# Kernel tuning notes

Hardware: AMD Instinct MI355X
Metric: run time of the kernel (lower is better)

## Reference

```python
import jax, jax.numpy as jnp
import numpy as np

B, T, N, M, P = 1024, 128, 128, 256, 256


def _lstm_step(x, h, c, Wih, Whh, bih, bhh):
    # PyTorch LSTM cell: gates ordered i, f, g, o
    g = x @ Wih.T + bih + h @ Whh.T + bhh
    i, f, gg, o = jnp.split(g, 4, axis=-1)
    c_new = jax.nn.sigmoid(f) * c + jax.nn.sigmoid(i) * jnp.tanh(gg)
    h_new = jax.nn.sigmoid(o) * jnp.tanh(c_new)
    return h_new, c_new


def darnn_forward(enc_data, dec_data, enc_Wih, enc_Whh, enc_bih, enc_bhh,
                  We, Ue, ve, Wd, Ud, vd, wt_w, wt_b,
                  dec_Wih, dec_Whh, dec_bih, dec_bhh, l1_w, l1_b, l2_w, l2_b):
    Bsz, Tlen, n = enc_data.shape
    m = enc_Whh.shape[1]
    p = dec_Whh.shape[1]
    # ---- Encoder with input attention ----
    # U_e(data.permute(0,2,1)): (B, n, T); constant across time steps
    Ue_data = jnp.einsum('btn,st->bns', enc_data, Ue)
    def enc_step(carry, x_t):
        h, c = carry                                   # (B, m) each
        q = jnp.concatenate([h, c], axis=-1)           # (B, 2m)
        wq = q @ We.T                                  # (B, T)
        score = jnp.tanh(wq[:, None, :] + Ue_data) @ ve  # (B, n)
        alpha = jax.nn.softmax(score, axis=-1)
        h, c = _lstm_step(alpha * x_t, h, c, enc_Wih, enc_Whh, enc_bih, enc_bhh)
        return (h, c), h
    h0 = jnp.zeros((Bsz, m), enc_data.dtype)
    (_, _), Hs = jax.lax.scan(enc_step, (h0, h0), jnp.swapaxes(enc_data, 0, 1))
    H = jnp.swapaxes(Hs, 0, 1)                         # (B, T, m)
    # ---- Decoder with temporal attention ----
    UH = jnp.einsum('btm,um->btu', H, Ud)              # (B, T, m); constant
    def attn_ctx(d, s):
        q = jnp.concatenate([d, s], axis=-1)           # (B, 2p)
        wq = q @ Wd.T                                  # (B, m)
        score = jnp.tanh(wq[:, None, :] + UH) @ vd     # (B, T)
        beta = jax.nn.softmax(score, axis=-1)
        return jnp.einsum('bt,btm->bm', beta, H)       # (B, m)
    def dec_step(carry, y):
        d, s = carry
        ctx = attn_ctx(d, s)
        y_tilde = jnp.concatenate([y, ctx], axis=-1) @ wt_w.T + wt_b  # (B, 1)
        d, s = _lstm_step(y_tilde, d, s, dec_Wih, dec_Whh, dec_bih, dec_bhh)
        return (d, s), None
    d0 = jnp.zeros((Bsz, p), enc_data.dtype)
    ys = jnp.swapaxes(dec_data[:, :Tlen - 1, :], 0, 1)  # (T-1, B, 1)
    (d, s), _ = jax.lax.scan(dec_step, (d0, d0), ys)
    ctx = attn_ctx(d, s)
    out = jnp.concatenate([d, ctx], axis=-1)            # (B, p + m)
    out = jax.nn.relu(out @ l1_w.T + l1_b) @ l2_w.T + l2_b
    return out.reshape(-1)


def setup_inputs() -> dict:
    key = jax.random.key(0)
    ks = jax.random.split(key, 22)
    f = lambda k, shape: jax.random.normal(k, shape, jnp.float32) * 0.05
    return {
        'enc_data': jax.random.normal(ks[0], (B, T, N), jnp.float32),
        'dec_data': jax.random.normal(ks[1], (B, T, 1), jnp.float32),
        'enc_Wih': f(ks[2], (4 * M, N)), 'enc_Whh': f(ks[3], (4 * M, M)),
        'enc_bih': f(ks[4], (4 * M,)), 'enc_bhh': f(ks[5], (4 * M,)),
        'We': f(ks[6], (T, 2 * M)), 'Ue': f(ks[7], (T, T)), 've': f(ks[8], (T,)),
        'Wd': f(ks[9], (M, 2 * P)), 'Ud': f(ks[10], (M, M)), 'vd': f(ks[11], (M,)),
        'wt_w': f(ks[12], (1, M + 1)), 'wt_b': f(ks[13], (1,)),
        'dec_Wih': f(ks[14], (4 * P, 1)), 'dec_Whh': f(ks[15], (4 * P, P)),
        'dec_bih': f(ks[16], (4 * P,)), 'dec_bhh': f(ks[17], (4 * P,)),
        'l1_w': f(ks[18], (P, M + P)), 'l1_b': f(ks[19], (P,)),
        'l2_w': f(ks[20], (1, P)), 'l2_b': f(ks[21], (1,)),
    }


def reference(enc_data, dec_data, enc_Wih, enc_Whh, enc_bih, enc_bhh,
              We, Ue, ve, Wd, Ud, vd, wt_w, wt_b,
              dec_Wih, dec_Whh, dec_bih, dec_bhh, l1_w, l1_b, l2_w, l2_b):
    return darnn_forward(enc_data, dec_data, enc_Wih, enc_Whh, enc_bih, enc_bhh,
                         We, Ue, ve, Wd, Ud, vd, wt_w, wt_b,
                         dec_Wih, dec_Whh, dec_bih, dec_bhh, l1_w, l1_b, l2_w, l2_b)
```

## Files before the change

### kernel.cpp

```cpp
#include <hip/hip_runtime.h>

typedef unsigned short ushort_t;
typedef unsigned char u8_t;
typedef float f32x2 __attribute__((ext_vector_type(2)));

static constexpr int BATCH = 1024;
static constexpr int TT = 128;
static constexpr int NN = 128;
static constexpr int MM = 256;

__device__ __forceinline__ float bf2f(ushort_t u) {
    union { unsigned int i; float f; } v;
    v.i = ((unsigned int)u) << 16;
    return v.f;
}
__device__ __forceinline__ ushort_t f2bf(float f) {
    union { unsigned int i; float f; } v;
    v.f = f;
    unsigned int i = v.i;
    return (ushort_t)((i + 0x7FFFu + ((i >> 16) & 1u)) >> 16);
}
__device__ __forceinline__ void unp8(const int4 w, float* o) {
    union { unsigned int i; float f; } v;
    v.i = ((unsigned int)w.x) << 16;        o[0] = v.f;
    v.i = ((unsigned int)w.x) & 0xffff0000u; o[1] = v.f;
    v.i = ((unsigned int)w.y) << 16;        o[2] = v.f;
    v.i = ((unsigned int)w.y) & 0xffff0000u; o[3] = v.f;
    v.i = ((unsigned int)w.z) << 16;        o[4] = v.f;
    v.i = ((unsigned int)w.z) & 0xffff0000u; o[5] = v.f;
    v.i = ((unsigned int)w.w) << 16;        o[6] = v.f;
    v.i = ((unsigned int)w.w) & 0xffff0000u; o[7] = v.f;
}
__device__ __forceinline__ void unp4(const int2 w, float* o) {
    union { unsigned int i; float f; } v;
    v.i = ((unsigned int)w.x) << 16;        o[0] = v.f;
    v.i = ((unsigned int)w.x) & 0xffff0000u; o[1] = v.f;
    v.i = ((unsigned int)w.y) << 16;        o[2] = v.f;
    v.i = ((unsigned int)w.y) & 0xffff0000u; o[3] = v.f;
}
__device__ __forceinline__ void unp8f8(const int2 w, float* o) {
    f32x2 a = __builtin_amdgcn_cvt_pk_f32_fp8(w.x, false);
    f32x2 b = __builtin_amdgcn_cvt_pk_f32_fp8(w.x, true);
    f32x2 c = __builtin_amdgcn_cvt_pk_f32_fp8(w.y, false);
    f32x2 d = __builtin_amdgcn_cvt_pk_f32_fp8(w.y, true);
    o[0] = a.x; o[1] = a.y; o[2] = b.x; o[3] = b.y;
    o[4] = c.x; o[5] = c.y; o[6] = d.x; o[7] = d.y;
}
__device__ __forceinline__ float tanh_fast(float x) {
    float e = __expf(2.0f * x);
    return 1.0f - __fdividef(2.0f, e + 1.0f);
}
__device__ __forceinline__ float sig_fast(float x) {
    return __fdividef(1.0f, 1.0f + __expf(-x));
}

template<bool WBF16, bool TRANSW, int CMODE, bool RELU>
__global__ __launch_bounds__(256) void gemm_k(
    const float* __restrict__ A1, int lda1, long sA1z, int K1,
    const float* __restrict__ A2, int lda2, int K2,
    const void* __restrict__ W1v, int ldw1, long sW1z,
    const void* __restrict__ W2v, int ldw2,
    const float* __restrict__ bias1,
    void* __restrict__ Cv, int ldc, long sCz)
{
    __shared__ float As[32][68];
    __shared__ float Ws[32][68];
    const int tid = threadIdx.x;
    const int z = blockIdx.z;
    const int m0 = blockIdx.y * 64;
    const int g0 = blockIdx.x * 64;
    const int tm = tid & 15, tn = tid >> 4;
    float acc[4][4];
#pragma unroll
    for (int i = 0; i < 4; ++i)
#pragma unroll
        for (int j = 0; j < 4; ++j) acc[i][j] = 0.0f;

    for (int phase = 0; phase < 2; ++phase) {
        const float* A = (phase == 0) ? (A1 + (long)z * sA1z) : A2;
        const int lda = (phase == 0) ? lda1 : lda2;
        const int K = (phase == 0) ? K1 : K2;
        const int ldw = (phase == 0) ? ldw1 : ldw2;
        const void* Wv = (phase == 0) ? W1v : W2v;
        const long woff = (phase == 0) ? (long)z * sW1z : 0;
        if (A == nullptr || Wv == nullptr || K <= 0) continue;

        for (int k0 = 0; k0 < K; k0 += 32) {
            const int rem = K - k0;
            {
                const int tr0 = tid >> 3;
                const int tk = (tid & 7) * 4;
#pragma unroll
                for (int pass = 0; pass < 2; ++pass) {
                    const int m = tr0 + pass * 32;
                    const float* p = A + (long)(m0 + m) * lda + k0 + tk;
#pragma unroll
                    for (int j = 0; j < 4; ++j) {
                        float v = 0.0f;
                        if (tk + j < rem) v = p[j];
                        As[tk + j][m] = v;
                    }
                }
            }
            if constexpr (TRANSW) {
                const float* W = (const float*)Wv + woff;
                const int gq = (tid & 15) * 4;
                const int kr = tid >> 4;
#pragma unroll
                for (int pass = 0; pass < 2; ++pass) {
                    const int k = kr + pass * 16;
                    const float* p = W + (long)(k0 + k) * ldw + g0 + gq;
                    const bool ok = (k < rem);
#pragma unroll
                    for (int j = 0; j < 4; ++j) {
                        float v = 0.0f;
                        if (ok) v = p[j];
                        Ws[k][gq + j] = v;
                    }
                }
            } else if constexpr (WBF16) {
                const ushort_t* W = (const ushort_t*)Wv + woff;
                const int g = tid >> 2;
                const int tk = (tid & 3) * 8;
                const ushort_t* p = W + (long)(g0 + g) * ldw + k0 + tk;
#pragma unroll
                for (int j = 0; j < 8; ++j) {
                    float v = 0.0f;
                    if (tk + j < rem) v = bf2f(p[j]);
                    Ws[tk + j][g] = v;
                }
            } else {
                const float* W = (const float*)Wv + woff;
                const int tr0 = tid >> 3;
                const int tk = (tid & 7) * 4;
#pragma unroll
                for (int pass = 0; pass < 2; ++pass) {
                    const int g = tr0 + pass * 32;
                    const float* p = W + (long)(g0 + g) * ldw + k0 + tk;
#pragma unroll
                    for (int j = 0; j < 4; ++j) {
                        float v = 0.0f;
                        if (tk + j < rem) v = p[j];
                        Ws[tk + j][g] = v;
                    }
                }
            }
            __syncthreads();
#pragma unroll
            for (int kk = 0; kk < 32; ++kk) {
                const float4 av = *(const float4*)&As[kk][tm * 4];
                const float4 bv = *(const float4*)&Ws[kk][tn * 4];
                const float a[4] = {av.x, av.y, av.z, av.w};
                const float b[4] = {bv.x, bv.y, bv.z, bv.w};
#pragma unroll
                for (int i = 0; i < 4; ++i)
#pragma unroll
                    for (int j = 0; j < 4; ++j)
                        acc[i][j] = fmaf(a[i], b[j], acc[i][j]);
            }
            __syncthreads();
        }
    }
#pragma unroll
    for (int i = 0; i < 4; ++i) {
        const long m = m0 + tm * 4 + i;
        if constexpr (CMODE == 2) {
            float v[4];
#pragma unroll
            for (int j = 0; j < 4; ++j) {
                v[j] = acc[i][j];
                if (bias1) v[j] += bias1[g0 + tn * 4 + j];
                if (RELU) v[j] = fmaxf(v[j], 0.0f);
            }
            int pk = __builtin_amdgcn_cvt_pk_fp8_f32(v[0], v[1], 0, false);
            pk = __builtin_amdgcn_cvt_pk_fp8_f32(v[2], v[3], pk, true);
            *(unsigned int*)((u8_t*)Cv + (long)z * sCz + m * ldc + g0 + tn * 4) =
                (unsigned int)pk;
        } else {
#pragma unroll
            for (int j = 0; j < 4; ++j) {
                const int g = g0 + tn * 4 + j;
                float v = acc[i][j];
                if (bias1) v += bias1[g];
                if (RELU) v = fmaxf(v, 0.0f);
                if constexpr (CMODE == 1)
                    ((ushort_t*)Cv)[(long)z * sCz + m * ldc + g] = f2bf(v);
                else
                    ((float*)Cv)[(long)z * sCz + m * ldc + g] = v;
            }
        }
    }
}

__global__ void prep_encw_k(const float* __restrict__ Wih, const float* __restrict__ Whh,
                            ushort_t* __restrict__ dst) {
    int i = blockIdx.x * 256 + threadIdx.x;
    if (i >= 384 * 1024) return;
    int k = i >> 10, col = i & 1023, u = col >> 2, q = col & 3, g = q * 256 + u;
    float v = (k < 128) ? Wih[g * 128 + k] : Whh[g * 256 + (k - 128)];
    dst[(k >> 1) * 2048 + u * 8 + (k & 1) * 4 + q] = f2bf(v);
}

__global__ void prep_decw_k(const float* __restrict__ Wih, const float* __restrict__ Whh,
                            ushort_t* __restrict__ dst) {
    int i = blockIdx.x * 256 + threadIdx.x;
    if (i >= 257 * 1024) return;
    int k = i >> 10, col = i & 1023, u = col >> 2, q = col & 3, g = q * 256 + u;
    float v = (k == 0) ? Wih[g] : Whh[g * 256 + (k - 1)];
    ushort_t b = f2bf(v);
    if (k == 0) {
        dst[col] = b;
    } else {
        int kk = k - 1;
        dst[1024 + (kk >> 1) * 2048 + u * 8 + (kk & 1) * 4 + q] = b;
    }
}

__global__ void transpose_k(const float* __restrict__ src, float* __restrict__ dst,
                            int R, int C) {
    int i = blockIdx.x * 256 + threadIdx.x;
    if (i < R * C) { int r = i / C, c = i - r * C; dst[c * R + r] = src[i]; }
}

__global__ void packT_k(const float* __restrict__ src, ushort_t* __restrict__ dst,
                        int R, int C) {
    int i = blockIdx.x * 256 + threadIdx.x;
    if (i >= R * C) return;
    int s = i / C, k = i - s * C;
    dst[(k >> 1) * (2 * R) + (s >> 2) * 8 + (k & 1) * 4 + (s & 3)] = f2bf(src[i]);
}

__global__ __launch_bounds__(512) void enc_persist(
    const float* __restrict__ enc_data,
    const u8_t* __restrict__ D,
    const ushort_t* __restrict__ WeB,
    const float* __restrict__ ve,
    const ushort_t* __restrict__ WencB,
    const float* __restrict__ bih, const float* __restrict__ bhh,
    ushort_t* __restrict__ Hbf)
{
    const int tid = threadIdx.x;
    const int b0 = blockIdx.x * 4;
    __shared__ __align__(16) float hs[256][4];
    __shared__ __align__(16) float cs[256][4];
    __shared__ __align__(16) float xt[128][4];
    __shared__ __align__(16) float wqp[16][128][4];
    __shared__ __align__(16) float wqs[128][4];
    __shared__ __align__(16) float scp[8][4][128];
    __shared__ float gp[4][4][256];
    __shared__ float ves[128];

    if (tid < 128) ves[tid] = ve[tid];
    if (tid < 256) {
        const float4 z = make_float4(0.f, 0.f, 0.f, 0.f);
        *(float4*)hs[tid] = z;
        *(float4*)cs[tid] = z;
    }
    const int u = tid & 255;
    const int ks = tid >> 8;
    const float b_i = bih[u] + bhh[u];
    const float b_f = bih[256 + u] + bhh[256 + u];
    const float b_g = bih[512 + u] + bhh[512 + u];
    const float b_o = bih[768 + u] + bhh[768 + u];
    __syncthreads();

    const int kgq = tid >> 5, sv = tid & 31;
    const ushort_t* wq_w = WeB + (long)(kgq * 16) * 256 + sv * 8;
    const float* qbase = (kgq < 8) ? &hs[kgq * 32][0] : &cs[(kgq - 8) * 32][0];
    const int nv = tid & 15, srow = (tid >> 4) & 3, ssl = tid >> 6;
    const u8_t* Dp0 = D + (long)(b0 + srow) * 16384 + (ssl * 16) * 128 + nv * 8;
    const ushort_t* gw = WencB + u * 8;

    float SVe = 0.0f;
#pragma unroll
    for (int s = 0; s < 16; ++s) SVe += ves[ssl * 16 + s];

    for (int t = 0; t < 128; ++t) {
        {
            float a[4][4];
#pragma unroll
            for (int m = 0; m < 4; ++m)
#pragma unroll
                for (int r = 0; r < 4; ++r) a[m][r] = 0.0f;
#pragma unroll 4
            for (int k2 = 0; k2 < 16; ++k2) {
                const int4 wv = *(const int4*)(wq_w + k2 * 256);
                float w8[8]; unp8(wv, w8);
                const float4 q0 = *(const float4*)(qbase + (2 * k2) * 4);
                const float4 q1 = *(const float4*)(qbase + (2 * k2 + 1) * 4);
                const float qa0[4] = {q0.x, q0.y, q0.z, q0.w};
                const float qa1[4] = {q1.x, q1.y, q1.z, q1.w};
#pragma unroll
                for (int m = 0; m < 4; ++m)
#pragma unroll
                    for (int r = 0; r < 4; ++r)
                        a[m][r] = fmaf(w8[4 + m], qa1[r], fmaf(w8[m], qa0[r], a[m][r]));
            }
#pragma unroll
            for (int m = 0; m < 4; ++m)
                *(float4*)wqp[kgq][sv * 4 + m] = make_float4(a[m][0], a[m][1], a[m][2], a[m][3]);
        }
        __syncthreads();
        if (tid < 128) {
            float4 s = *(const float4*)wqp[0][tid];
#pragma unroll
            for (int g = 1; g < 16; ++g) {
                const float4 p = *(const float4*)wqp[g][tid];
                s.x += p.x; s.y += p.y; s.z += p.z; s.w += p.w;
            }
            *(float4*)wqs[tid] = s;
        }
        __syncthreads();
        {
            float a[8];
#pragma unroll
            for (int j = 0; j < 8; ++j) a[j] = 0.0f;
#pragma unroll 4
            for (int s = 0; s < 16; ++s) {
                const int sg = ssl * 16 + s;
                const float w2 = wqs[sg][srow] * 2.0f;
                const float vv = ves[sg];
                const int2 wv2 = *(const int2*)(Dp0 + s * 128);
                float d[8];
                unp8f8(wv2, d);
#pragma unroll
                for (int j = 0; j < 8; ++j) {
                    const float ex = __expf(fmaf(d[j], 2.0f, w2));
                    a[j] = fmaf(vv, __fdividef(1.0f, ex + 1.0f), a[j]);
                }
            }
            *(float4*)&scp[ssl][srow][nv * 8] =
                make_float4(fmaf(-2.f, a[0], SVe), fmaf(-2.f, a[1], SVe),
                            fmaf(-2.f, a[2], SVe), fmaf(-2.f, a[3], SVe));
            *(float4*)&scp[ssl][srow][nv * 8 + 4] =
                make_float4(fmaf(-2.f, a[4], SVe), fmaf(-2.f, a[5], SVe),
                            fmaf(-2.f, a[6], SVe), fmaf(-2.f, a[7], SVe));
        }
        __syncthreads();
        if (tid < 256) {
            const int w = tid >> 6, lane = tid & 63;
            float s0 = 0.0f, s1 = 0.0f;
#pragma unroll
            for (int g = 0; g < 8; ++g) {
                s0 += scp[g][w][lane];
                s1 += scp[g][w][lane + 64];
            }
            float mx = fmaxf(s0, s1);
            for (int o = 32; o > 0; o >>= 1) mx = fmaxf(mx, __shfl_xor(mx, o, 64));
            const float e0 = __expf(s0 - mx), e1 = __expf(s1 - mx);
            float sm = e0 + e1;
            for (int o = 32; o > 0; o >>= 1) sm += __shfl_xor(sm, o, 64);
            const float inv = __fdividef(1.0f, sm);
            const float* xp = enc_data + ((long)(b0 + w) * 128 + t) * 128;
            xt[lane][w] = e0 * inv * xp[lane];
            xt[lane + 64][w] = e1 * inv * xp[lane + 64];
        }
        __syncthreads();
        float acc[4][4];
#pragma unroll
        for (int q = 0; q < 4; ++q)
#pragma unroll
            for (int r = 0; r < 4; ++r) acc[q][r] = 0.0f;
        if (ks == 0) {
#pragma unroll 4
            for (int p = 0; p < 64; ++p) {
                const int4 wv = *(const int4*)(gw + (long)p * 2048);
                float w8[8]; unp8(wv, w8);
                const float4 x0 = *(const float4*)xt[2 * p];
                const float4 x1 = *(const float4*)xt[2 * p + 1];
                const float xa0[4] = {x0.x, x0.y, x0.z, x0.w};
                const float xa1[4] = {x1.x, x1.y, x1.z, x1.w};
#pragma unroll
                for (int q = 0; q < 4; ++q)
#pragma unroll
                    for (int r = 0; r < 4; ++r)
                        acc[q][r] = fmaf(w8[4 + q], xa1[r], fmaf(w8[q], xa0[r], acc[q][r]));
            }
#pragma unroll 4
            for (int p = 64; p < 96; ++p) {
                const int4 wv = *(const int4*)(gw + (long)p * 2048);
                float w8[8]; unp8(wv, w8);
                const float4 x0 = *(const float4*)hs[2 * p - 128];
                const float4 x1 = *(const float4*)hs[2 * p - 127];
                const float xa0[4] = {x0.x, x0.y, x0.z, x0.w};
                const float xa1[4] = {x1.x, x1.y, x1.z, x1.w};
#pragma unroll
                for (int q = 0; q < 4; ++q)
#pragma unroll
                    for (int r = 0; r < 4; ++r)
                        acc[q][r] = fmaf(w8[4 + q], xa1[r], fmaf(w8[q], xa0[r], acc[q][r]));
            }
        } else {
#pragma unroll 4
            for (int p = 96; p < 192; ++p) {
                const int4 wv = *(const int4*)(gw + (long)p * 2048);
                float w8[8]; unp8(wv, w8);
                const float4 x0 = *(const float4*)hs[2 * p - 128];
                const float4 x1 = *(const float4*)hs[2 * p - 127];
                const float xa0[4] = {x0.x, x0.y, x0.z, x0.w};
                const float xa1[4] = {x1.x, x1.y, x1.z, x1.w};
#pragma unroll
                for (int q = 0; q < 4; ++q)
#pragma unroll
                    for (int r = 0; r < 4; ++r)
                        acc[q][r] = fmaf(w8[4 + q], xa1[r], fmaf(w8[q], xa0[r], acc[q][r]));
            }
#pragma unroll
            for (int q = 0; q < 4; ++q)
#pragma unroll
                for (int r = 0; r < 4; ++r) gp[q][r][u] = acc[q][r];
        }
        __syncthreads();
        if (ks == 0) {
#pragma unroll
            for (int r = 0; r < 4; ++r) {
                const float iv = sig_fast(acc[0][r] + gp[0][r][u] + b_i);
                const float fv = sig_fast(acc[1][r] + gp[1][r][u] + b_f);
                const float gv = tanh_fast(acc[2][r] + gp[2][r][u] + b_g);
                const float ov = sig_fast(acc[3][r] + gp[3][r][u] + b_o);
                const float cn = fv * cs[u][r] + iv * gv;
                const float hn = ov * tanh_fast(cn);
                cs[u][r] = cn;
                hs[u][r] = hn;
                Hbf[((long)(b0 + r) * 128 + t) * 256 + u] = f2bf(hn);
            }
        }
        __syncthreads();
    }
}

__global__ __launch_bounds__(512) void dec_persist(
    const float* __restrict__ dec_data,
    const u8_t* __restrict__ UH2,
    const ushort_t* __restrict__ Hb,
    const ushort_t* __restrict__ WdB,
    const float* __restrict__ vd,
    const ushort_t* __restrict__ WdecB,
    const float* __restrict__ bih, const float* __restrict__ bhh,
    const float* __restrict__ wt_w, const float* __restrict__ wt_b,
    const float* __restrict__ l1T,
    const float* __restrict__ l1_b,
    const float* __restrict__ l2_w, const float* __restrict__ l2_b,
    float* __restrict__ out)
{
    const int tid = threadIdx.x;
    const int b0 = blockIdx.x * 4;
    __shared__ __align__(16) float ds4[256][4];
    __shared__ __align__(16) float ss4[256][4];
    __shared__ __align__(16) float wqp[8][256][4];
    __shared__ __align__(16) float wqs[256][4];
    __shared__ __align__(16) float scp[8][4][128];
    __shared__ __align__(16) float beta[128][4];
    __shared__ __align__(16) float ctxp[4][4][256];
    __shared__ __align__(16) float ctx4[256][4];
    __shared__ float gp[4][4][256];
    __shared__ __align__(16) float o14[256][4];
    __shared__ float vds[256];
    __shared__ float wt1s[256];
    __shared__ float l2s[256];
    __shared__ __align__(16) float yts[4];

    const int u = tid & 255;
    const int ks = tid >> 8;
    if (tid < 256) {
        vds[tid] = vd[tid];
        wt1s[tid] = wt_w[1 + tid];
        l2s[tid] = l2_w[tid];
        const float4 z = make_float4(0.f, 0.f, 0.f, 0.f);
        *(float4*)ds4[tid] = z;
        *(float4*)ss4[tid] = z;
    }
    const float b_i = bih[u] + bhh[u];
    const float b_f = bih[256 + u] + bhh[256 + u];
    const float b_g = bih[512 + u] + bhh[512 + u];
    const float b_o = bih[768 + u] + bhh[768 + u];
    __syncthreads();

    const int kgq = tid >> 6, mv = tid & 63;
    const ushort_t* wq_w = WdB + (long)(kgq * 32) * 512 + mv * 8;
    const float* qbase = (kgq < 4) ? &ds4[kgq * 64][0] : &ss4[(kgq - 4) * 64][0];
    const int tv = tid & 15, srow = (tid >> 4) & 3, usl = tid >> 6;
    const u8_t* up0 = UH2 + ((long)(b0 + srow) * 256 + usl * 32) * 128 + tv * 8;
    const int mv8 = tid & 31, crow = (tid >> 5) & 3, ssl2 = tid >> 7;
    const ushort_t* hp0 = Hb + ((long)(b0 + crow) * 128 + ssl2 * 32) * 256 + mv8 * 8;
    const ushort_t* gwp = WdecB + 1024 + u * 8;

    float SVd = 0.0f;
#pragma unroll
    for (int s = 0; s < 32; ++s) SVd += vds[usl * 32 + s];

    for (int td = 0; td < 128; ++td) {
        {
            float a[4][4];
#pragma unroll
            for (int m = 0; m < 4; ++m)
#pragma unroll
                for (int r = 0; r < 4; ++r) a[m][r] = 0.0f;
#pragma unroll 4
            for (int k2 = 0; k2 < 32; ++k2) {
                const int4 wv = *(const int4*)(wq_w + k2 * 512);
                float w8[8]; unp8(wv, w8);
                const float4 q0 = *(const float4*)(qbase + (2 * k2) * 4);
                const float4 q1 = *(const float4*)(qbase + (2 * k2 + 1) * 4);
                const float qa0[4] = {q0.x, q0.y, q0.z, q0.w};
                const float qa1[4] = {q1.x, q1.y, q1.z, q1.w};
#pragma unroll
                for (int m = 0; m < 4; ++m)
#pragma unroll
                    for (int r = 0; r < 4; ++r)
                        a[m][r] = fmaf(w8[4 + m], qa1[r], fmaf(w8[m], qa0[r], a[m][r]));
            }
#pragma unroll
            for (int m = 0; m < 4; ++m)
                *(float4*)wqp[kgq][mv * 4 + m] = make_float4(a[m][0], a[m][1], a[m][2], a[m][3]);
        }
        __syncthreads();
        if (tid < 256) {
            float4 s = *(const float4*)wqp[0][tid];
#pragma unroll
            for (int g = 1; g < 8; ++g) {
                const float4 p = *(const float4*)wqp[g][tid];
                s.x += p.x; s.y += p.y; s.z += p.z; s.w += p.w;
            }
            *(float4*)wqs[tid] = s;
        }
        __syncthreads();
        {
            float a[8];
#pragma unroll
            for (int j = 0; j < 8; ++j) a[j] = 0.0f;
#pragma unroll 4
            for (int uu = 0; uu < 32; ++uu) {
                const int ug = usl * 32 + uu;
                const float w2 = wqs[ug][srow] * 2.0f;
                const float vv = vds[ug];
                const int2 wv2 = *(const int2*)(up0 + uu * 128);
                float d[8];
                unp8f8(wv2, d);
#pragma unroll
                for (int j = 0; j < 8; ++j) {
                    const float ex = __expf(fmaf(d[j], 2.0f, w2));
                    a[j] = fmaf(vv, __fdividef(1.0f, ex + 1.0f), a[j]);
                }
            }
            *(float4*)&scp[usl][srow][tv * 8] =
                make_float4(fmaf(-2.f, a[0], SVd), fmaf(-2.f, a[1], SVd),
                            fmaf(-2.f, a[2], SVd), fmaf(-2.f, a[3], SVd));
            *(float4*)&scp[usl][srow][tv * 8 + 4] =
                make_float4(fmaf(-2.f, a[4], SVd), fmaf(-2.f, a[5], SVd),
                            fmaf(-2.f, a[6], SVd), fmaf(-2.f, a[7], SVd));
        }
        __syncthreads();
        if (tid < 256) {
            const int w = tid >> 6, lane = tid & 63;
            float s0 = 0.0f, s1 = 0.0f;
#pragma unroll
            for (int g = 0; g < 8; ++g) {
                s0 += scp[g][w][lane];
                s1 += scp[g][w][lane + 64];
            }
            float mx = fmaxf(s0, s1);
            for (int o = 32; o > 0; o >>= 1) mx = fmaxf(mx, __shfl_xor(mx, o, 64));
            const float e0 = __expf(s0 - mx), e1 = __expf(s1 - mx);
            float sm = e0 + e1;
            for (int o = 32; o > 0; o >>= 1) sm += __shfl_xor(sm, o, 64);
            const float inv = __fdividef(1.0f, sm);
            beta[lane][w] = e0 * inv;
            beta[lane + 64][w] = e1 * inv;
        }
        __syncthreads();
        {
            float c[8];
#pragma unroll
            for (int j = 0; j < 8; ++j) c[j] = 0.0f;
#pragma unroll 4
            for (int s = 0; s < 32; ++s) {
                const float bt = beta[ssl2 * 32 + s][crow];
                const int4 wv2 = *(const int4*)(hp0 + s * 256);
                float hv[8];
                unp8(wv2, hv);
#pragma unroll
                for (int j = 0; j < 8; ++j)
                    c[j] = fmaf(bt, hv[j], c[j]);
            }
            *(float4*)&ctxp[ssl2][crow][mv8 * 8]     = make_float4(c[0], c[1], c[2], c[3]);
            *(float4*)&ctxp[ssl2][crow][mv8 * 8 + 4] = make_float4(c[4], c[5], c[6], c[7]);
        }
        __syncthreads();
        if (tid < 256) {
            const int m = tid;
            float cr[4];
#pragma unroll
            for (int r = 0; r < 4; ++r)
                cr[r] = ctxp[0][r][m] + ctxp[1][r][m] + ctxp[2][r][m] + ctxp[3][r][m];
            *(float4*)ctx4[m] = make_float4(cr[0], cr[1], cr[2], cr[3]);
        }
        __syncthreads();
        if (td == 127) break;
        if (tid < 256) {
            const int w = tid >> 6, lane = tid & 63;
            float s = ctx4[lane][w] * wt1s[lane]
                    + ctx4[lane + 64][w] * wt1s[lane + 64]
                    + ctx4[lane + 128][w] * wt1s[lane + 128]
                    + ctx4[lane + 192][w] * wt1s[lane + 192];
            for (int o = 32; o > 0; o >>= 1) s += __shfl_xor(s, o, 64);
            if (lane == 0)
                yts[w] = s + wt_b[0] + wt_w[0] * dec_data[(long)(b0 + w) * 128 + td];
        }
        __syncthreads();
        float acc[4][4];
        if (ks == 0) {
            const int2 yv = *(const int2*)(WdecB + u * 4);
            float wy[4]; unp4(yv, wy);
            const float4 y4 = *(const float4*)yts;
            const float ya[4] = {y4.x, y4.y, y4.z, y4.w};
#pragma unroll
            for (int q = 0; q < 4; ++q)
#pragma unroll
                for (int r = 0; r < 4; ++r) acc[q][r] = wy[q] * ya[r];
#pragma unroll 4
            for (int p = 0; p < 64; ++p) {
                const int4 wv = *(const int4*)(gwp + (long)p * 2048);
                float w8[8]; unp8(wv, w8);
                const float4 x0 = *(const float4*)ds4[2 * p];
                const float4 x1 = *(const float4*)ds4[2 * p + 1];
                const float xa0[4] = {x0.x, x0.y, x0.z, x0.w};
                const float xa1[4] = {x1.x, x1.y, x1.z, x1.w};
#pragma unroll
                for (int q = 0; q < 4; ++q)
#pragma unroll
                    for (int r = 0; r < 4; ++r)
                        acc[q][r] = fmaf(w8[4 + q], xa1[r], fmaf(w8[q], xa0[r], acc[q][r]));
            }
        } else {
#pragma unroll
            for (int q = 0; q < 4; ++q)
#pragma unroll
                for (int r = 0; r < 4; ++r) acc[q][r] = 0.0f;
#pragma unroll 4
            for (int p = 64; p < 128; ++p) {
                const int4 wv = *(const int4*)(gwp + (long)p * 2048);
                float w8[8]; unp8(wv, w8);
                const float4 x0 = *(const float4*)ds4[2 * p];
                const float4 x1 = *(const float4*)ds4[2 * p + 1];
                const float xa0[4] = {x0.x, x0.y, x0.z, x0.w};
                const float xa1[4] = {x1.x, x1.y, x1.z, x1.w};
#pragma unroll
                for (int q = 0; q < 4; ++q)
#pragma unroll
                    for (int r = 0; r < 4; ++r)
                        acc[q][r] = fmaf(w8[4 + q], xa1[r], fmaf(w8[q], xa0[r], acc[q][r]));
            }
#pragma unroll
            for (int q = 0; q < 4; ++q)
#pragma unroll
                for (int r = 0; r < 4; ++r) gp[q][r][u] = acc[q][r];
        }
        __syncthreads();
        if (ks == 0) {
#pragma unroll
            for (int r = 0; r < 4; ++r) {
                const float iv = sig_fast(acc[0][r] + gp[0][r][u] + b_i);
                const float fv = sig_fast(acc[1][r] + gp[1][r][u] + b_f);
                const float gv = tanh_fast(acc[2][r] + gp[2][r][u] + b_g);
                const float ov = sig_fast(acc[3][r] + gp[3][r][u] + b_o);
                const float sn = fv * ss4[u][r] + iv * gv;
                const float dn = ov * tanh_fast(sn);
                ss4[u][r] = sn;
                ds4[u][r] = dn;
            }
        }
        __syncthreads();
    }
    {
        const float* src = l1T + ks * 256 * 256;
        float a0 = 0, a1 = 0, a2 = 0, a3 = 0;
#pragma unroll 4
        for (int k = 0; k < 256; ++k) {
            const float w = src[k * 256 + u];
            const float4 q = (ks == 0) ? *(const float4*)ds4[k]
                                       : *(const float4*)ctx4[k];
            a0 = fmaf(q.x, w, a0); a1 = fmaf(q.y, w, a1);
            a2 = fmaf(q.z, w, a2); a3 = fmaf(q.w, w, a3);
        }
        if (ks == 1) {
            gp[0][0][u] = a0; gp[0][1][u] = a1; gp[0][2][u] = a2; gp[0][3][u] = a3;
        } else {
            gp[1][0][u] = a0; gp[1][1][u] = a1; gp[1][2][u] = a2; gp[1][3][u] = a3;
        }
    }
    __syncthreads();
    if (tid < 256) {
        const float bb = l1_b[tid];
        *(float4*)o14[tid] = make_float4(
            fmaxf(gp[0][0][tid] + gp[1][0][tid] + bb, 0.f),
            fmaxf(gp[0][1][tid] + gp[1][1][tid] + bb, 0.f),
            fmaxf(gp[0][2][tid] + gp[1][2][tid] + bb, 0.f),
            fmaxf(gp[0][3][tid] + gp[1][3][tid] + bb, 0.f));
    }
    __syncthreads();
    if (tid < 256) {
        const int w = tid >> 6, lane = tid & 63;
        float s = o14[lane][w] * l2s[lane]
                + o14[lane + 64][w] * l2s[lane + 64]
                + o14[lane + 128][w] * l2s[lane + 128]
                + o14[lane + 192][w] * l2s[lane + 192];
        for (int o = 32; o > 0; o >>= 1) s += __shfl_xor(s, o, 64);
        if (lane == 0) out[b0 + w] = s + l2_b[0];
    }
}

extern "C" void kernel_launch(void* const* d_in, const int* in_sizes, int n_in,
                              void* d_out, int out_size, void* d_ws, size_t ws_size,
                              hipStream_t stream)
{
    const float* enc_data = (const float*)d_in[0];
    const float* dec_data = (const float*)d_in[1];
    const float* enc_Wih  = (const float*)d_in[2];
    const float* enc_Whh  = (const float*)d_in[3];
    const float* enc_bih  = (const float*)d_in[4];
    const float* enc_bhh  = (const float*)d_in[5];
    const float* We   = (const float*)d_in[6];
    const float* Ue   = (const float*)d_in[7];
    const float* ve   = (const float*)d_in[8];
    const float* Wd   = (const float*)d_in[9];
    const float* Ud   = (const float*)d_in[10];
    const float* vd   = (const float*)d_in[11];
    const float* wt_w = (const float*)d_in[12];
    const float* wt_b = (const float*)d_in[13];
    const float* dec_Wih = (const float*)d_in[14];
    const float* dec_Whh = (const float*)d_in[15];
    const float* dec_bih = (const float*)d_in[16];
    const float* dec_bhh = (const float*)d_in[17];
    const float* l1_w = (const float*)d_in[18];
    const float* l1_b = (const float*)d_in[19];
    const float* l2_w = (const float*)d_in[20];
    const float* l2_b = (const float*)d_in[21];

    ushort_t* Hbf  = (ushort_t*)d_ws;
    u8_t* Dbf      = (u8_t*)(Hbf + (long)BATCH * TT * MM);
    u8_t* UHbf     = Dbf + (long)BATCH * TT * NN;
    ushort_t* WencB = (ushort_t*)(UHbf + (long)BATCH * MM * TT);
    ushort_t* WdecB = WencB + 384 * 1024;
    ushort_t* WeB   = WdecB + 257 * 1024;
    ushort_t* WdB   = WeB + 512 * 128;
    float* l1T      = (float*)(WdB + 512 * 256);

    prep_encw_k<<<1536, 256, 0, stream>>>(enc_Wih, enc_Whh, WencB);
    prep_decw_k<<<1028, 256, 0, stream>>>(dec_Wih, dec_Whh, WdecB);
    packT_k<<<(128 * 512 + 255) / 256, 256, 0, stream>>>(We, WeB, 128, 512);
    packT_k<<<(256 * 512 + 255) / 256, 256, 0, stream>>>(Wd, WdB, 256, 512);
    transpose_k<<<(256 * 512 + 255) / 256, 256, 0, stream>>>(l1_w, l1T, 256, 512);

    gemm_k<false, true, 2, false><<<dim3(NN / 64, TT / 64, BATCH), 256, 0, stream>>>(
        Ue, TT, 0, TT,
        nullptr, 0, 0,
        enc_data, NN, (long)TT * NN,
        nullptr, 0,
        nullptr,
        Dbf, NN, (long)TT * NN);

    enc_persist<<<256, 512, 0, stream>>>(enc_data, Dbf, WeB, ve, WencB,
                                         enc_bih, enc_bhh, Hbf);

    gemm_k<true, false, 2, false><<<dim3(TT / 64, MM / 64, BATCH), 256, 0, stream>>>(
        Ud, MM, 0, MM,
        nullptr, 0, 0,
        Hbf, MM, (long)TT * MM,
        nullptr, 0,
        nullptr,
        UHbf, TT, (long)MM * TT);

    dec_persist<<<256, 512, 0, stream>>>(dec_data, UHbf, Hbf, WdB, vd, WdecB,
                                         dec_bih, dec_bhh, wt_w, wt_b,
                                         l1T, l1_b, l2_w, l2_b, (float*)d_out);
}
```

Baseline: 9.896 ms.

## Use v_dot2_f32_bf16 for recurrent matvecs with bf16-packed state and interleaved weights

Weight packing now interleaves adjacent-k bf16 pairs, and the LSTM hidden/cell state and attended inputs are stored in shared memory as packed bf16 pairs. The inner matvec loops use the v_dot2_f32_bf16 instruction, which replaces two FMAs plus the unpack shifts for each pair. This cuts VALU work and shared-memory traffic in the sequential encoder and decoder steps. In exchange the activations (h, c, d, s, the attended x) are rounded to bf16 before each matvec, which lowers accuracy.

```diff
diff --git a/kernel.cpp b/kernel.cpp
--- a/kernel.cpp
+++ b/kernel.cpp
@@ -2,6 +2,7 @@
 
 typedef unsigned short ushort_t;
 typedef unsigned char u8_t;
+typedef unsigned int u32_t;
 typedef float f32x2 __attribute__((ext_vector_type(2)));
 
 static constexpr int BATCH = 1024;
@@ -19,6 +20,14 @@
     v.f = f;
     unsigned int i = v.i;
     return (ushort_t)((i + 0x7FFFu + ((i >> 16) & 1u)) >> 16);
+}
+__device__ __forceinline__ u32_t pk2bf(float lo, float hi) {
+    return (u32_t)f2bf(lo) | ((u32_t)f2bf(hi) << 16);
+}
+__device__ __forceinline__ float dot2bf(u32_t a, u32_t b, float c) {
+    float d;
+    asm("v_dot2_f32_bf16 %0, %1, %2, %3" : "=v"(d) : "v"(a), "v"(b), "v"(c));
+    return d;
 }
 __device__ __forceinline__ void unp8(const int4 w, float* o) {
     union { unsigned int i; float f; } v;
@@ -198,7 +207,7 @@
     if (i >= 384 * 1024) return;
     int k = i >> 10, col = i & 1023, u = col >> 2, q = col & 3, g = q * 256 + u;
     float v = (k < 128) ? Wih[g * 128 + k] : Whh[g * 256 + (k - 128)];
-    dst[(k >> 1) * 2048 + u * 8 + (k & 1) * 4 + q] = f2bf(v);
+    dst[(k >> 1) * 2048 + u * 8 + q * 2 + (k & 1)] = f2bf(v);
 }
 
 __global__ void prep_decw_k(const float* __restrict__ Wih, const float* __restrict__ Whh,
@@ -212,7 +221,7 @@
         dst[col] = b;
     } else {
         int kk = k - 1;
-        dst[1024 + (kk >> 1) * 2048 + u * 8 + (kk & 1) * 4 + q] = b;
+        dst[1024 + (kk >> 1) * 2048 + u * 8 + q * 2 + (kk & 1)] = b;
     }
 }
 
@@ -227,7 +236,7 @@
     int i = blockIdx.x * 256 + threadIdx.x;
     if (i >= R * C) return;
     int s = i / C, k = i - s * C;
-    dst[(k >> 1) * (2 * R) + (s >> 2) * 8 + (k & 1) * 4 + (s & 3)] = f2bf(src[i]);
+    dst[(k >> 1) * (2 * R) + (s >> 2) * 8 + (s & 3) * 2 + (k & 1)] = f2bf(src[i]);
 }
 
 __global__ __launch_bounds__(512) void enc_persist(
@@ -241,9 +250,9 @@
 {
     const int tid = threadIdx.x;
     const int b0 = blockIdx.x * 4;
-    __shared__ __align__(16) float hs[256][4];
     __shared__ __align__(16) float cs[256][4];
-    __shared__ __align__(16) float xt[128][4];
+    __shared__ __align__(16) u32_t qpk[256][4];
+    __shared__ __align__(16) u32_t xtp[64][4];
     __shared__ __align__(16) float wqp[16][128][4];
     __shared__ __align__(16) float wqs[128][4];
     __shared__ __align__(16) float scp[8][4][128];
@@ -253,8 +262,11 @@
     if (tid < 128) ves[tid] = ve[tid];
     if (tid < 256) {
         const float4 z = make_float4(0.f, 0.f, 0.f, 0.f);
-        *(float4*)hs[tid] = z;
         *(float4*)cs[tid] = z;
+    }
+    {
+        uint4 z4 = {0u, 0u, 0u, 0u};
+        for (int i = tid; i < 256; i += 512) *(uint4*)qpk[i] = z4;
     }
     const int u = tid & 255;
     const int ks = tid >> 8;
@@ -266,7 +278,6 @@
 
     const int kgq = tid >> 5, sv = tid & 31;
     const ushort_t* wq_w = WeB + (long)(kgq * 16) * 256 + sv * 8;
-    const float* qbase = (kgq < 8) ? &hs[kgq * 32][0] : &cs[(kgq - 8) * 32][0];
     const int nv = tid & 15, srow = (tid >> 4) & 3, ssl = tid >> 6;
     const u8_t* Dp0 = D + (long)(b0 + srow) * 16384 + (ssl * 16) * 128 + nv * 8;
     const ushort_t* gw = WencB + u * 8;
@@ -284,17 +295,15 @@
                 for (int r = 0; r < 4; ++r) a[m][r] = 0.0f;
 #pragma unroll 4
             for (int k2 = 0; k2 < 16; ++k2) {
-                const int4 wv = *(const int4*)(wq_w + k2 * 256);
-                float w8[8]; unp8(wv, w8);
-                const float4 q0 = *(const float4*)(qbase + (2 * k2) * 4);
-                const float4 q1 = *(const float4*)(qbase + (2 * k2 + 1) * 4);
-                const float qa0[4] = {q0.x, q0.y, q0.z, q0.w};
-                const float qa1[4] = {q1.x, q1.y, q1.z, q1.w};
+                const uint4 wv = *(const uint4*)(wq_w + k2 * 256);
+                const uint4 qv = *(const uint4*)qpk[kgq * 16 + k2];
+                const u32_t wa[4] = {wv.x, wv.y, wv.z, wv.w};
+                const u32_t qa[4] = {qv.x, qv.y, qv.z, qv.w};
 #pragma unroll
                 for (int m = 0; m < 4; ++m)
 #pragma unroll
                     for (int r = 0; r < 4; ++r)
-                        a[m][r] = fmaf(w8[4 + m], qa1[r], fmaf(w8[m], qa0[r], a[m][r]));
+                        a[m][r] = dot2bf(wa[m], qa[r], a[m][r]);
             }
 #pragma unroll
             for (int m = 0; m < 4; ++m)
@@ -352,8 +361,14 @@
             for (int o = 32; o > 0; o >>= 1) sm += __shfl_xor(sm, o, 64);
             const float inv = __fdividef(1.0f, sm);
             const float* xp = enc_data + ((long)(b0 + w) * 128 + t) * 128;
-            xt[lane][w] = e0 * inv * xp[lane];
-            xt[lane + 64][w] = e1 * inv * xp[lane + 64];
+            const float v0 = e0 * inv * xp[lane];
+            const float v1 = e1 * inv * xp[lane + 64];
+            const float p0 = __shfl_xor(v0, 1, 64);
+            const float p1 = __shfl_xor(v1, 1, 64);
+            if ((lane & 1) == 0) {
+                xtp[lane >> 1][w] = pk2bf(v0, p0);
+                xtp[32 + (lane >> 1)][w] = pk2bf(v1, p1);
+            }
         }
         __syncthreads();
         float acc[4][4];
@@ -364,46 +379,40 @@
         if (ks == 0) {
 #pragma unroll 4
             for (int p = 0; p < 64; ++p) {
-                const int4 wv = *(const int4*)(gw + (long)p * 2048);
-                float w8[8]; unp8(wv, w8);
-                const float4 x0 = *(const float4*)xt[2 * p];
-                const float4 x1 = *(const float4*)xt[2 * p + 1];
-                const float xa0[4] = {x0.x, x0.y, x0.z, x0.w};
-                const float xa1[4] = {x1.x, x1.y, x1.z, x1.w};
+                const uint4 wv = *(const uint4*)(gw + (long)p * 2048);
+                const uint4 xv = *(const uint4*)xtp[p];
+                const u32_t wa[4] = {wv.x, wv.y, wv.z, wv.w};
+                const u32_t xa[4] = {xv.x, xv.y, xv.z, xv.w};
 #pragma unroll
                 for (int q = 0; q < 4; ++q)
 #pragma unroll
                     for (int r = 0; r < 4; ++r)
-                        acc[q][r] = fmaf(w8[4 + q], xa1[r], fmaf(w8[q], xa0[r], acc[q][r]));
+                        acc[q][r] = dot2bf(wa[q], xa[r], acc[q][r]);
             }
 #pragma unroll 4
             for (int p = 64; p < 96; ++p) {
-                const int4 wv = *(const int4*)(gw + (long)p * 2048);
-                float w8[8]; unp8(wv, w8);
-                const float4 x0 = *(const float4*)hs[2 * p - 128];
-                const float4 x1 = *(const float4*)hs[2 * p - 127];
-                const float xa0[4] = {x0.x, x0.y, x0.z, x0.w};
-                const float xa1[4] = {x1.x, x1.y, x1.z, x1.w};
+                const uint4 wv = *(const uint4*)(gw + (long)p * 2048);
+                const uint4 xv = *(const uint4*)qpk[p - 64];
+                const u32_t wa[4] = {wv.x, wv.y, wv.z, wv.w};
+                const u32_t xa[4] = {xv.x, xv.y, xv.z, xv.w};
 #pragma unroll
                 for (int q = 0; q < 4; ++q)
 #pragma unroll
                     for (int r = 0; r < 4; ++r)
-                        acc[q][r] = fmaf(w8[4 + q], xa1[r], fmaf(w8[q], xa0[r], acc[q][r]));
+                        acc[q][r] = dot2bf(wa[q], xa[r], acc[q][r]);
             }
         } else {
 #pragma unroll 4
             for (int p = 96; p < 192; ++p) {
-                const int4 wv = *(const int4*)(gw + (long)p * 2048);
-                float w8[8]; unp8(wv, w8);
-                const float4 x0 = *(const float4*)hs[2 * p - 128];
-                const float4 x1 = *(const float4*)hs[2 * p - 127];
-                const float xa0[4] = {x0.x, x0.y, x0.z, x0.w};
-                const float xa1[4] = {x1.x, x1.y, x1.z, x1.w};
+                const uint4 wv = *(const uint4*)(gw + (long)p * 2048);
+                const uint4 xv = *(const uint4*)qpk[p - 64];
+                const u32_t wa[4] = {wv.x, wv.y, wv.z, wv.w};
+                const u32_t xa[4] = {xv.x, xv.y, xv.z, xv.w};
 #pragma unroll
                 for (int q = 0; q < 4; ++q)
 #pragma unroll
                     for (int r = 0; r < 4; ++r)
-                        acc[q][r] = fmaf(w8[4 + q], xa1[r], fmaf(w8[q], xa0[r], acc[q][r]));
+                        acc[q][r] = dot2bf(wa[q], xa[r], acc[q][r]);
             }
 #pragma unroll
             for (int q = 0; q < 4; ++q)
@@ -421,7 +430,12 @@
                 const float cn = fv * cs[u][r] + iv * gv;
                 const float hn = ov * tanh_fast(cn);
                 cs[u][r] = cn;
-                hs[u][r] = hn;
+                const float hp = __shfl_xor(hn, 1, 64);
+                const float cp = __shfl_xor(cn, 1, 64);
+                if ((u & 1) == 0) {
+                    qpk[u >> 1][r] = pk2bf(hn, hp);
+                    qpk[128 + (u >> 1)][r] = pk2bf(cn, cp);
+                }
                 Hbf[((long)(b0 + r) * 128 + t) * 256 + u] = f2bf(hn);
             }
         }
@@ -447,6 +461,7 @@
     const int b0 = blockIdx.x * 4;
     __shared__ __align__(16) float ds4[256][4];
     __shared__ __align__(16) float ss4[256][4];
+    __shared__ __align__(16) u32_t qpk[256][4];
     __shared__ __align__(16) float wqp[8][256][4];
     __shared__ __align__(16) float wqs[256][4];
     __shared__ __align__(16) float scp[8][4][128];
@@ -470,6 +485,10 @@
         *(float4*)ds4[tid] = z;
         *(float4*)ss4[tid] = z;
     }
+    {
+        uint4 z4 = {0u, 0u, 0u, 0u};
+        for (int i = tid; i < 256; i += 512) *(uint4*)qpk[i] = z4;
+    }
     const float b_i = bih[u] + bhh[u];
     const float b_f = bih[256 + u] + bhh[256 + u];
     const float b_g = bih[512 + u] + bhh[512 + u];
@@ -478,7 +497,6 @@
 
     const int kgq = tid >> 6, mv = tid & 63;
     const ushort_t* wq_w = WdB + (long)(kgq * 32) * 512 + mv * 8;
-    const float* qbase = (kgq < 4) ? &ds4[kgq * 64][0] : &ss4[(kgq - 4) * 64][0];
     const int tv = tid & 15, srow = (tid >> 4) & 3, usl = tid >> 6;
     const u8_t* up0 = UH2 + ((long)(b0 + srow) * 256 + usl * 32) * 128 + tv * 8;
     const int mv8 = tid & 31, crow = (tid >> 5) & 3, ssl2 = tid >> 7;
@@ -498,17 +516,15 @@
                 for (int r = 0; r < 4; ++r) a[m][r] = 0.0f;
 #pragma unroll 4
             for (int k2 = 0; k2 < 32; ++k2) {
-                const int4 wv = *(const int4*)(wq_w + k2 * 512);
-                float w8[8]; unp8(wv, w8);
-                const float4 q0 = *(const float4*)(qbase + (2 * k2) * 4);
-                const float4 q1 = *(const float4*)(qbase + (2 * k2 + 1) * 4);
-                const float qa0[4] = {q0.x, q0.y, q0.z, q0.w};
-                const float qa1[4] = {q1.x, q1.y, q1.z, q1.w};
+                const uint4 wv = *(const uint4*)(wq_w + k2 * 512);
+                const uint4 qv = *(const uint4*)qpk[kgq * 32 + k2];
+                const u32_t wa[4] = {wv.x, wv.y, wv.z, wv.w};
+                const u32_t qa[4] = {qv.x, qv.y, qv.z, qv.w};
 #pragma unroll
                 for (int m = 0; m < 4; ++m)
 #pragma unroll
                     for (int r = 0; r < 4; ++r)
-                        a[m][r] = fmaf(w8[4 + m], qa1[r], fmaf(w8[m], qa0[r], a[m][r]));
+                        a[m][r] = dot2bf(wa[m], qa[r], a[m][r]);
             }
 #pragma unroll
             for (int m = 0; m < 4; ++m)
@@ -620,17 +636,15 @@
                 for (int r = 0; r < 4; ++r) acc[q][r] = wy[q] * ya[r];
 #pragma unroll 4
             for (int p = 0; p < 64; ++p) {
-                const int4 wv = *(const int4*)(gwp + (long)p * 2048);
-                float w8[8]; unp8(wv, w8);
-                const float4 x0 = *(const float4*)ds4[2 * p];
-                const float4 x1 = *(const float4*)ds4[2 * p + 1];
-                const float xa0[4] = {x0.x, x0.y, x0.z, x0.w};
-                const float xa1[4] = {x1.x, x1.y, x1.z, x1.w};
+                const uint4 wv = *(const uint4*)(gwp + (long)p * 2048);
+                const uint4 xv = *(const uint4*)qpk[p];
+                const u32_t wa[4] = {wv.x, wv.y, wv.z, wv.w};
+                const u32_t xa[4] = {xv.x, xv.y, xv.z, xv.w};
 #pragma unroll
                 for (int q = 0; q < 4; ++q)
 #pragma unroll
                     for (int r = 0; r < 4; ++r)
-                        acc[q][r] = fmaf(w8[4 + q], xa1[r], fmaf(w8[q], xa0[r], acc[q][r]));
+                        acc[q][r] = dot2bf(wa[q], xa[r], acc[q][r]);
             }
         } else {
 #pragma unroll
@@ -639,17 +653,15 @@
                 for (int r = 0; r < 4; ++r) acc[q][r] = 0.0f;
 #pragma unroll 4
             for (int p = 64; p < 128; ++p) {
-                const int4 wv = *(const int4*)(gwp + (long)p * 2048);
-                float w8[8]; unp8(wv, w8);
-                const float4 x0 = *(const float4*)ds4[2 * p];
-                const float4 x1 = *(const float4*)ds4[2 * p + 1];
-                const float xa0[4] = {x0.x, x0.y, x0.z, x0.w};
-                const float xa1[4] = {x1.x, x1.y, x1.z, x1.w};
+                const uint4 wv = *(const uint4*)(gwp + (long)p * 2048);
+                const uint4 xv = *(const uint4*)qpk[p];
+                const u32_t wa[4] = {wv.x, wv.y, wv.z, wv.w};
+                const u32_t xa[4] = {xv.x, xv.y, xv.z, xv.w};
 #pragma unroll
                 for (int q = 0; q < 4; ++q)
 #pragma unroll
                     for (int r = 0; r < 4; ++r)
-                        acc[q][r] = fmaf(w8[4 + q], xa1[r], fmaf(w8[q], xa0[r], acc[q][r]));
+                        acc[q][r] = dot2bf(wa[q], xa[r], acc[q][r]);
             }
 #pragma unroll
             for (int q = 0; q < 4; ++q)
@@ -668,6 +680,12 @@
                 const float dn = ov * tanh_fast(sn);
                 ss4[u][r] = sn;
                 ds4[u][r] = dn;
+                const float dp = __shfl_xor(dn, 1, 64);
+                const float sp = __shfl_xor(sn, 1, 64);
+                if ((u & 1) == 0) {
+                    qpk[u >> 1][r] = pk2bf(dn, dp);
+                    qpk[128 + (u >> 1)][r] = pk2bf(sn, sp);
+                }
             }
         }
         __syncthreads();
```

New measurement: 9.415 ms. 4.9% less time.
